# Optimization experiments

Measured on AMD Instinct MI355X. Metric: run time of the kernel, lower is better.

The kernel has to match this reference:

```python
import jax, jax.numpy as jnp
import numpy as np

NX = 496
NY = 496
C = 64
B = 4
P = 12000


def setup_inputs() -> dict:
    key = jax.random.key(0)
    k1, k2 = jax.random.split(key)
    pillar_features = jax.random.normal(k1, (B, P, C), dtype=jnp.float32)
    coords = jax.random.randint(k2, (B, P, 3), 0, 496, dtype=jnp.int32)
    return {"pillar_features": pillar_features, "coords": coords}


def reference(pillar_features, coords):
    # pillar_features: (B, P, C) float; coords: (B, P, 3) int [batch_idx, x_idx, y_idx]
    b, p, c = pillar_features.shape
    x = coords[:, :, 1]
    y = coords[:, :, 2]
    # module masks pillars where x_idx + y_idx > 0, then bounds-checks indices
    valid = ((x + y) > 0) & (x >= 0) & (x < NX) & (y >= 0) & (y < NY)
    batch_ids = jnp.arange(b, dtype=coords.dtype)[:, None]  # (B, 1)
    flat_idx = batch_ids * (NX * NY) + x * NY + y            # (B, P)
    dump = b * NX * NY  # extra slot for invalid pillars
    flat_idx = jnp.where(valid, flat_idx, dump)
    buf = jnp.zeros((b * NX * NY + 1, c), dtype=pillar_features.dtype)
    buf = buf.at[flat_idx.reshape(-1)].set(pillar_features.reshape(-1, c))
    bev = buf[:-1].reshape(b, NX, NY, c).transpose(0, 3, 1, 2)  # (B, C, NX, NY)
    return bev
```

## Files before the change

kernel.cpp:

```cpp
#include <hip/hip_runtime.h>


#define NXD 496
#define NYD 496
#define CD  64
#define BD  4
#define PD  12000
#define NXNY (NXD * NYD)
#define NY4 (NYD / 4)
#define CBLK 16
#define NCB (CD / CBLK)

__global__ void pp_init_winner(int* __restrict__ winner) {
    const int total4 = BD * NXNY / 4;
    int tid = blockIdx.x * blockDim.x + threadIdx.x;
    if (tid < total4) {
        reinterpret_cast<int4*>(winner)[tid] = make_int4(-1, -1, -1, -1);
    }
}

__global__ void pp_scatter_idx(const int* __restrict__ coords,
                               int* __restrict__ winner) {
    int tid = blockIdx.x * blockDim.x + threadIdx.x;
    if (tid >= BD * PD) return;
    int b = tid / PD;
    int x = coords[tid * 3 + 1];
    int y = coords[tid * 3 + 2];
    bool valid = (x + y > 0) && (x >= 0) && (x < NXD) && (y >= 0) && (y < NYD);
    if (valid) {
        int p = tid - b * PD;
        atomicMax(&winner[b * NXNY + x * NYD + y], p);
    }
}

__global__ void pp_gather_out(const float* __restrict__ feats,
                              const int* __restrict__ winner,
                              float* __restrict__ out) {
    const int total = BD * NXD * NY4;
    int tid = blockIdx.x * blockDim.x + threadIdx.x;
    if (tid >= total) return;

    int y4 = tid % NY4;
    int r  = tid / NY4;
    int x  = r % NXD;
    int b  = r / NXD;

    const int4 w = *reinterpret_cast<const int4*>(
        &winner[b * NXNY + x * NYD + y4 * 4]);
    const int wa[4] = { w.x, w.y, w.z, w.w };

    const float* fb = feats + (size_t)b * PD * CD;
    float* obase = out + (((size_t)b * CD * NXD + x) * NYD + y4 * 4);

#pragma unroll
    for (int cb = 0; cb < NCB; ++cb) {
        float f[4][CBLK] = {};

#pragma unroll
        for (int j = 0; j < 4; ++j) {
            if (wa[j] >= 0) {
                const float4* src = reinterpret_cast<const float4*>(
                    fb + (size_t)wa[j] * CD + cb * CBLK);
                float4 a0 = src[0], a1 = src[1], a2 = src[2], a3 = src[3];
                f[j][0]  = a0.x; f[j][1]  = a0.y; f[j][2]  = a0.z; f[j][3]  = a0.w;
                f[j][4]  = a1.x; f[j][5]  = a1.y; f[j][6]  = a1.z; f[j][7]  = a1.w;
                f[j][8]  = a2.x; f[j][9]  = a2.y; f[j][10] = a2.z; f[j][11] = a2.w;
                f[j][12] = a3.x; f[j][13] = a3.y; f[j][14] = a3.z; f[j][15] = a3.w;
            }
        }

#pragma unroll
        for (int c = 0; c < CBLK; ++c) {
            float4 v = make_float4(f[0][c], f[1][c], f[2][c], f[3][c]);
            *reinterpret_cast<float4*>(
                obase + (size_t)(cb * CBLK + c) * NXNY) = v;
        }
    }
}

extern "C" void kernel_launch(void* const* d_in, const int* in_sizes, int n_in,
                              void* d_out, int out_size, void* d_ws, size_t ws_size,
                              hipStream_t stream) {
    const float* feats  = (const float*)d_in[0];
    const int*   coords = (const int*)d_in[1];
    float*       out    = (float*)d_out;
    int*         winner = (int*)d_ws;

    const int init4 = BD * NXNY / 4;
    pp_init_winner<<<(init4 + 255) / 256, 256, 0, stream>>>(winner);

    pp_scatter_idx<<<(BD * PD + 255) / 256, 256, 0, stream>>>(coords, winner);

    const int total = BD * NXD * NY4;
    pp_gather_out<<<(total + 255) / 256, 256, 0, stream>>>(feats, winner, out);
}
```

Baseline: 52.90 us.

## Drop winner-buffer init by validating stale indices against pillar coords

Removes the kernel that fills the winner map with -1. Stale or garbage entries left in the workspace are instead checked against the current coords: scatter uses a CAS loop that only keeps an old index if that pillar really maps to the cell and has a higher index, and gather re-checks each winner's coords before reading features. This saves a full pass of writes over the winner map, at the cost of extra coord loads and CAS retries in both scatter and gather.

```diff
diff --git a/kernel.cpp b/kernel.cpp
--- a/kernel.cpp
+++ b/kernel.cpp
@@ -11,14 +11,6 @@
 #define CBLK 16
 #define NCB (CD / CBLK)
 
-__global__ void pp_init_winner(int* __restrict__ winner) {
-    const int total4 = BD * NXNY / 4;
-    int tid = blockIdx.x * blockDim.x + threadIdx.x;
-    if (tid < total4) {
-        reinterpret_cast<int4*>(winner)[tid] = make_int4(-1, -1, -1, -1);
-    }
-}
-
 __global__ void pp_scatter_idx(const int* __restrict__ coords,
                                int* __restrict__ winner) {
     int tid = blockIdx.x * blockDim.x + threadIdx.x;
@@ -27,13 +19,25 @@
     int x = coords[tid * 3 + 1];
     int y = coords[tid * 3 + 2];
     bool valid = (x + y > 0) && (x >= 0) && (x < NXD) && (y >= 0) && (y < NYD);
-    if (valid) {
-        int p = tid - b * PD;
-        atomicMax(&winner[b * NXNY + x * NYD + y], p);
+    if (!valid) return;
+
+    int p = tid - b * PD;
+    int* cell = &winner[b * NXNY + x * NYD + y];
+    const int* cb = coords + (size_t)b * PD * 3;
+
+    int old = atomicCAS(cell, -1, p);
+    while (old != -1) {
+        bool oldClaims = (old >= 0) && (old < PD) &&
+                         (cb[old * 3 + 1] == x) && (cb[old * 3 + 2] == y);
+        if (oldClaims && old >= p) break;
+        int assumed = old;
+        old = atomicCAS(cell, assumed, p);
+        if (old == assumed) break;
     }
 }
 
 __global__ void pp_gather_out(const float* __restrict__ feats,
+                              const int* __restrict__ coords,
                               const int* __restrict__ winner,
                               float* __restrict__ out) {
     const int total = BD * NXD * NY4;
@@ -44,13 +48,26 @@
     int r  = tid / NY4;
     int x  = r % NXD;
     int b  = r / NXD;
+    int y0 = y4 * 4;
 
     const int4 w = *reinterpret_cast<const int4*>(
-        &winner[b * NXNY + x * NYD + y4 * 4]);
-    const int wa[4] = { w.x, w.y, w.z, w.w };
+        &winner[b * NXNY + x * NYD + y0]);
+    int wa[4] = { w.x, w.y, w.z, w.w };
+
+    const int* cbase = coords + (size_t)b * PD * 3;
+#pragma unroll
+    for (int j = 0; j < 4; ++j) {
+        int v = wa[j];
+        bool ok = (v >= 0) && (v < PD);
+        if (ok) {
+            ok = (cbase[v * 3 + 1] == x) && (cbase[v * 3 + 2] == y0 + j) &&
+                 (x + y0 + j > 0);
+        }
+        wa[j] = ok ? v : -1;
+    }
 
     const float* fb = feats + (size_t)b * PD * CD;
-    float* obase = out + (((size_t)b * CD * NXD + x) * NYD + y4 * 4);
+    float* obase = out + (((size_t)b * CD * NXD + x) * NYD + y0);
 
 #pragma unroll
     for (int cb = 0; cb < NCB; ++cb) {
@@ -86,11 +103,8 @@
     float*       out    = (float*)d_out;
     int*         winner = (int*)d_ws;
 
-    const int init4 = BD * NXNY / 4;
-    pp_init_winner<<<(init4 + 255) / 256, 256, 0, stream>>>(winner);
-
     pp_scatter_idx<<<(BD * PD + 255) / 256, 256, 0, stream>>>(coords, winner);
 
     const int total = BD * NXD * NY4;
-    pp_gather_out<<<(total + 255) / 256, 256, 0, stream>>>(feats, winner, out);
+    pp_gather_out<<<(total + 255) / 256, 256, 0, stream>>>(feats, coords, winner, out);
 }
```

Result: faster. 48.67 us (-8.0%).
